# Kernel optimization log

Hardware: AMD Instinct MI355X
Metric: run time of the kernel (lower is better)

Reference implementation:

```python
import jax, jax.numpy as jnp
import numpy as np

EMBED_DIM = 768
N_HEADS = 12
HEAD_DIM = EMBED_DIM // N_HEADS


def setup_inputs() -> dict:
    key = jax.random.key(0)
    ks = jax.random.split(key, 5)
    B, T, C = 2, 4096, EMBED_DIM
    x = jax.random.normal(ks[0], (B, T, C), dtype=jnp.float32)
    # nn.Linear default init scale ~ 1/sqrt(fan_in); use small-scale normals
    s = 1.0 / np.sqrt(C)
    W_qkv = jax.random.normal(ks[1], (C, 3 * C), dtype=jnp.float32) * s
    b_qkv = jax.random.normal(ks[2], (3 * C,), dtype=jnp.float32) * s
    W_proj = jax.random.normal(ks[3], (C, C), dtype=jnp.float32) * s
    b_proj = jax.random.normal(ks[4], (C,), dtype=jnp.float32) * s
    return {"x": x, "W_qkv": W_qkv, "b_qkv": b_qkv, "W_proj": W_proj, "b_proj": b_proj}


def reference(x, W_qkv, b_qkv, W_proj, b_proj):
    B, T, C = x.shape
    H, D = N_HEADS, HEAD_DIM
    qkv = x @ W_qkv + b_qkv                      # [B,T,3C]
    q, k, v = jnp.split(qkv, 3, axis=2)
    # [B,T,C] -> [B,H,T,D]
    q = q.reshape(B, T, H, D).transpose(0, 2, 1, 3)
    k = k.reshape(B, T, H, D).transpose(0, 2, 1, 3)
    v = v.reshape(B, T, H, D).transpose(0, 2, 1, 3)
    scale = 1.0 / jnp.sqrt(jnp.float32(D)).astype(x.dtype)
    attn = jnp.einsum('bhtd,bhsd->bhts', q, k) * scale   # [B,H,T,T]
    causal = jnp.tril(jnp.ones((T, T), dtype=bool))
    attn = jnp.where(causal, attn, jnp.float32(-jnp.inf).astype(attn.dtype))
    attn = jax.nn.softmax(attn, axis=-1)
    # dropout p=0.0 -> identity
    out = jnp.einsum('bhts,bhsd->bhtd', attn, v)          # [B,H,T,D]
    out = out.transpose(0, 2, 1, 3).reshape(B, T, C)
    return out @ W_proj + b_proj
```

## Files before the change

### kernel.cpp

```cpp
#include <hip/hip_runtime.h>
#include <math.h>

#define T_SEQ 4096
#define CDIM  768
#define NH    12
#define HD    64
#define BATCH 2
#define MROWS (BATCH * T_SEQ)
#define N3C   (3 * CDIM)
#define HEADS_TOTAL (BATCH * NH)
#define QKV_ELEMS   ((size_t)HEADS_TOTAL * T_SEQ * HD)

#define QSCALE 0.18033688011112042f
#define SSHIFT -12.0f

typedef __bf16 bf16x8 __attribute__((ext_vector_type(8)));
typedef __bf16 bf16x4 __attribute__((ext_vector_type(4)));
typedef __bf16 bf16x2 __attribute__((ext_vector_type(2)));
typedef float  f32x4  __attribute__((ext_vector_type(4)));
typedef short  s16x4  __attribute__((ext_vector_type(4)));

union b4u { bf16x4 h; s16x4 s; };
__device__ __forceinline__ s16x4 as_s16(bf16x4 v) { b4u u; u.h = v; return u.s; }

typedef __attribute__((address_space(1))) const void as1_cvoid;
typedef __attribute__((address_space(3))) void as3_void;

__device__ __forceinline__ void gl16(const void* g, void* l) {
  __builtin_amdgcn_global_load_lds((as1_cvoid*)g, (as3_void*)l, 16, 0, 0);
}

__global__ __launch_bounds__(256) void cast_x_kernel(
    const float* __restrict__ x, __bf16* __restrict__ xb) {
  int i = (blockIdx.x * 256 + threadIdx.x) * 8;
  float4 a = *(const float4*)&x[i];
  float4 b = *(const float4*)&x[i + 4];
  bf16x8 o;
  o[0] = (__bf16)a.x; o[1] = (__bf16)a.y; o[2] = (__bf16)a.z; o[3] = (__bf16)a.w;
  o[4] = (__bf16)b.x; o[5] = (__bf16)b.y; o[6] = (__bf16)b.z; o[7] = (__bf16)b.w;
  *(bf16x8*)&xb[i] = o;
}

__global__ __launch_bounds__(256) void tcast_kernel(
    const float* __restrict__ W, __bf16* __restrict__ Wt, int K, int N) {
  __shared__ float tile[64][65];
  const int t  = threadIdx.x;
  const int k0 = blockIdx.y * 64, n0 = blockIdx.x * 64;
  const int r  = t >> 4, c4 = (t & 15) << 2;
#pragma unroll
  for (int i = 0; i < 4; ++i) {
    float4 v = *(const float4*)&W[(size_t)(k0 + r + i * 16) * N + n0 + c4];
    tile[r + i * 16][c4 + 0] = v.x; tile[r + i * 16][c4 + 1] = v.y;
    tile[r + i * 16][c4 + 2] = v.z; tile[r + i * 16][c4 + 3] = v.w;
  }
  __syncthreads();
#pragma unroll
  for (int i = 0; i < 4; ++i) {
    int nr = r + i * 16;
    bf16x4 o;
    o[0] = (__bf16)tile[c4 + 0][nr]; o[1] = (__bf16)tile[c4 + 1][nr];
    o[2] = (__bf16)tile[c4 + 2][nr]; o[3] = (__bf16)tile[c4 + 3][nr];
    *(bf16x4*)&Wt[(size_t)(n0 + nr) * K + k0 + c4] = o;
  }
}

__device__ __forceinline__ void mm_loop(const __bf16* __restrict__ A,
                                        const __bf16* __restrict__ Bt,
                                        int m0, int n0, __bf16* smem,
                                        f32x4 acc[4][4]) {
  const int t = threadIdx.x, wv = t >> 6, lane = t & 63;
  const int g2 = lane >> 4, c = lane & 15;
  __bf16* At = smem;
  __bf16* Bs = smem + 4096;
  const int ch0 = wv * 64 + lane;
  const int ch1 = 256 + ch0;
  const __bf16* gA0 = A  + (size_t)(m0 + (ch0 >> 2)) * CDIM + ((ch0 & 3) << 3);
  const __bf16* gA1 = A  + (size_t)(m0 + (ch1 >> 2)) * CDIM + ((ch1 & 3) << 3);
  const __bf16* gB0 = Bt + (size_t)(n0 + (ch0 >> 2)) * CDIM + ((ch0 & 3) << 3);
  const __bf16* gB1 = Bt + (size_t)(n0 + (ch1 >> 2)) * CDIM + ((ch1 & 3) << 3);
  __bf16* lA0 = At + (size_t)(wv * 64) * 8;
  __bf16* lA1 = At + (size_t)(256 + wv * 64) * 8;
  __bf16* lB0 = Bs + (size_t)(wv * 64) * 8;
  __bf16* lB1 = Bs + (size_t)(256 + wv * 64) * 8;
  const int mw = (wv & 1) << 6, nw = (wv >> 1) << 6;

  for (int kk = 0; kk < CDIM / 32; ++kk) {
    __syncthreads();
    gl16(gA0, lA0); gl16(gA1, lA1);
    gl16(gB0, lB0); gl16(gB1, lB1);
    gA0 += 32; gA1 += 32; gB0 += 32; gB1 += 32;
    __syncthreads();
    bf16x8 af[4], bfr[4];
#pragma unroll
    for (int mq = 0; mq < 4; ++mq)
      af[mq] = *(const bf16x8*)&At[(size_t)(mw + mq * 16 + c) * 32 + (g2 << 3)];
#pragma unroll
    for (int nq = 0; nq < 4; ++nq)
      bfr[nq] = *(const bf16x8*)&Bs[(size_t)(nw + nq * 16 + c) * 32 + (g2 << 3)];
#pragma unroll
    for (int mq = 0; mq < 4; ++mq)
#pragma unroll
      for (int nq = 0; nq < 4; ++nq)
        acc[mq][nq] = __builtin_amdgcn_mfma_f32_16x16x32_bf16(
            af[mq], bfr[nq], acc[mq][nq], 0, 0, 0);
  }
  __syncthreads();
}

__global__ __launch_bounds__(256) void qkv_mm_kernel(
    const __bf16* __restrict__ xb, const __bf16* __restrict__ Wt,
    const float* __restrict__ bias, __bf16* __restrict__ Qw,
    __bf16* __restrict__ Kw, __bf16* __restrict__ Vtw) {
  __shared__ __align__(16) __bf16 smem[18432];
  f32x4 acc[4][4];
#pragma unroll
  for (int i = 0; i < 4; ++i)
#pragma unroll
    for (int j = 0; j < 4; ++j) acc[i][j] = (f32x4){0.f, 0.f, 0.f, 0.f};

  const int m0 = blockIdx.y * 128, n0 = blockIdx.x * 128;
  mm_loop(xb, Wt, m0, n0, smem, acc);

  const int t = threadIdx.x, wv = t >> 6, lane = t & 63;
  const int g2 = lane >> 4, c = lane & 15;
  const int sel = n0 / CDIM;
  const int nn0 = n0 - sel * CDIM;
  const int h   = (nn0 >> 6) + (wv >> 1);
  const int mbase = m0 + ((wv & 1) << 6);
  const int b = mbase >> 12, tp0 = mbase & 4095;
  const int bh = b * NH + h;
  __bf16* Ep = smem + wv * 4608;
  float bcol[4];
#pragma unroll
  for (int nq = 0; nq < 4; ++nq)
    bcol[nq] = bias[n0 + ((wv >> 1) << 6) + nq * 16 + c];

  const int r8 = lane >> 3, c8 = (lane & 7) << 3;
  if (sel < 2) {
    const float scl = (sel == 0) ? QSCALE : 1.0f;
#pragma unroll
    for (int mq = 0; mq < 4; ++mq)
#pragma unroll
      for (int nq = 0; nq < 4; ++nq)
#pragma unroll
        for (int r = 0; r < 4; ++r)
          Ep[(size_t)(mq * 16 + (g2 << 2) + r) * 72 + nq * 16 + c] =
              (__bf16)((acc[mq][nq][r] + bcol[nq]) * scl);
    asm volatile("s_waitcnt lgkmcnt(0)" ::: "memory");
    __bf16* dst = (sel == 0) ? Qw : Kw;
#pragma unroll
    for (int p = 0; p < 8; ++p) {
      int row = p * 8 + r8;
      bf16x8 v = *(const bf16x8*)&Ep[(size_t)row * 72 + c8];
      *(bf16x8*)&dst[((size_t)bh * T_SEQ + tp0 + row) * HD + c8] = v;
    }
  } else {
#pragma unroll
    for (int mq = 0; mq < 4; ++mq)
#pragma unroll
      for (int nq = 0; nq < 4; ++nq)
#pragma unroll
        for (int r = 0; r < 4; ++r)
          Ep[(size_t)(nq * 16 + c) * 72 + mq * 16 + (g2 << 2) + r] =
              (__bf16)(acc[mq][nq][r] + bcol[nq]);
    asm volatile("s_waitcnt lgkmcnt(0)" ::: "memory");
#pragma unroll
    for (int p = 0; p < 8; ++p) {
      int d = p * 8 + r8;
      bf16x8 v = *(const bf16x8*)&Ep[(size_t)d * 72 + c8];
      *(bf16x8*)&Vtw[((size_t)bh * HD + d) * T_SEQ + tp0 + c8] = v;
    }
  }
}

struct Stage { bf16x8 k0, k1, v0, v1; };

__device__ __forceinline__ void issue_stage(const __bf16* __restrict__ Kb,
                                            const __bf16* __restrict__ Vb,
                                            int kt, int wv, int lane, Stage& sg) {
  const int r8 = lane >> 3;
  const int cc = (lane & 7) << 3;
  const int row0 = (wv << 4) + r8;
  const int row1 = row0 + 8;
  sg.k0 = *(const bf16x8*)&Kb[(size_t)(kt * 64 + row0) * HD + cc];
  sg.k1 = *(const bf16x8*)&Kb[(size_t)(kt * 64 + row1) * HD + cc];
  sg.v0 = *(const bf16x8*)&Vb[(size_t)row0 * T_SEQ + kt * 64 + cc];
  sg.v1 = *(const bf16x8*)&Vb[(size_t)row1 * T_SEQ + kt * 64 + cc];
}

__device__ __forceinline__ void write_stage(__bf16 (*KT)[64], __bf16 (*VT)[64],
                                            int wv, int lane, const Stage& sg) {
  const int r8 = lane >> 3;
  const int cc = ((lane & 7) << 3) ^ (r8 << 3);
  const int row0 = (wv << 4) + r8;
  const int row1 = row0 + 8;
  *(bf16x8*)&KT[row0][cc] = sg.k0;
  *(bf16x8*)&KT[row1][cc] = sg.k1;
  *(bf16x8*)&VT[row0][cc] = sg.v0;
  *(bf16x8*)&VT[row1][cc] = sg.v1;
}

__global__ __launch_bounds__(256) void attn_kernel(
    const __bf16* __restrict__ Q, const __bf16* __restrict__ K,
    const __bf16* __restrict__ Vt, __bf16* __restrict__ O) {
  __shared__ __align__(16) __bf16 KT[2][64][64];
  __shared__ __align__(16) __bf16 VT[2][64][64];

  const int t    = threadIdx.x;
  const int wv   = t >> 6;
  const int lane = t & 63;
  const int g2   = lane >> 4;
  const int c    = lane & 15;
  const int bh   = blockIdx.x;
  const int qt   = 63 - (int)blockIdx.y;

  const __bf16* Qb = Q  + (size_t)bh * T_SEQ * HD;
  const __bf16* Kb = K  + (size_t)bh * T_SEQ * HD;
  const __bf16* Vb = Vt + (size_t)bh * HD * T_SEQ;
  const int b = bh / NH, hh = bh % NH;

  const int qw = qt * 64 + wv * 16;

  bf16x8 qf0 = *(const bf16x8*)&Qb[(size_t)(qw + c) * HD +      (g2 << 3)];
  bf16x8 qf1 = *(const bf16x8*)&Qb[(size_t)(qw + c) * HD + 32 + (g2 << 3)];

  f32x4 ot[4];
#pragma unroll
  for (int dt = 0; dt < 4; ++dt) ot[dt] = (f32x4){0.f, 0.f, 0.f, 0.f};
  f32x4 lacc = (f32x4){0.f, 0.f, 0.f, 0.f};

  Stage sg;
  issue_stage(Kb, Vb, 0, wv, lane, sg);
  write_stage(KT[0], VT[0], wv, lane, sg);
  __syncthreads();

  const int swz = (c & 7) << 3;

#pragma unroll 1
  for (int kt = 0; kt <= qt; ++kt) {
    const int cur = kt & 1;
    if (kt < qt) issue_stage(Kb, Vb, kt + 1, wv, lane, sg);

    f32x4 S[4];
#pragma unroll
    for (int st = 0; st < 4; ++st) {
      bf16x8 kfa = *(const bf16x8*)&KT[cur][st * 16 + c][(g2 << 3) ^ swz];
      bf16x8 kfb = *(const bf16x8*)&KT[cur][st * 16 + c][((g2 << 3) + 32) ^ swz];
      S[st] = (f32x4){SSHIFT, SSHIFT, SSHIFT, SSHIFT};
      S[st] = __builtin_amdgcn_mfma_f32_16x16x32_bf16(kfa, qf0, S[st], 0, 0, 0);
      S[st] = __builtin_amdgcn_mfma_f32_16x16x32_bf16(kfb, qf1, S[st], 0, 0, 0);
    }

    if (kt == qt) {
      const int qloc = (wv << 4) + c;
#pragma unroll
      for (int st = 0; st < 4; ++st)
#pragma unroll
        for (int r = 0; r < 4; ++r)
          if ((st << 4) + (g2 << 2) + r > qloc) S[st][r] = -INFINITY;
    }

    s16x4 pf[4];
#pragma unroll
    for (int st = 0; st < 4; ++st) {
      bf16x4 ph;
#pragma unroll
      for (int r = 0; r < 4; ++r) {
        float p = exp2f(S[st][r]);
        lacc[r] += p;
        ph[r] = (__bf16)p;
      }
      pf[st] = as_s16(ph);
    }

#pragma unroll
    for (int dt = 0; dt < 4; ++dt) {
#pragma unroll
      for (int st = 0; st < 4; ++st) {
        bf16x4 vh = *(const bf16x4*)&VT[cur][dt * 16 + c]
                                       [((st << 4) + (g2 << 2)) ^ swz];
        ot[dt] = __builtin_amdgcn_mfma_f32_16x16x16bf16_1k(
            as_s16(vh), pf[st], ot[dt], 0, 0, 0);
      }
    }

    if (kt < qt) write_stage(KT[cur ^ 1], VT[cur ^ 1], wv, lane, sg);
    __syncthreads();
  }

  float l = lacc[0] + lacc[1] + lacc[2] + lacc[3];
  l += __shfl_xor(l, 16);
  l += __shfl_xor(l, 32);
  const float inv = 1.f / l;
  __bf16* orow = O + ((size_t)(b * T_SEQ + qw + c)) * CDIM + hh * HD;
#pragma unroll
  for (int dt = 0; dt < 4; ++dt) {
    bf16x4 v;
    v[0] = (__bf16)(ot[dt][0] * inv); v[1] = (__bf16)(ot[dt][1] * inv);
    v[2] = (__bf16)(ot[dt][2] * inv); v[3] = (__bf16)(ot[dt][3] * inv);
    *(bf16x4*)&orow[dt * 16 + (g2 << 2)] = v;
  }
}

__global__ __launch_bounds__(256) void proj_mm_kernel(
    const __bf16* __restrict__ Ob, const __bf16* __restrict__ Wt,
    const float* __restrict__ bias, float* __restrict__ out) {
  __shared__ __align__(16) __bf16 smem[8192];
  f32x4 acc[4][4];
#pragma unroll
  for (int i = 0; i < 4; ++i)
#pragma unroll
    for (int j = 0; j < 4; ++j) acc[i][j] = (f32x4){0.f, 0.f, 0.f, 0.f};

  const int m0 = blockIdx.y * 128, n0 = blockIdx.x * 128;
  mm_loop(Ob, Wt, m0, n0, smem, acc);

  const int t = threadIdx.x, wv = t >> 6, lane = t & 63;
  const int g2 = lane >> 4, c = lane & 15;
  const int mb = m0 + ((wv & 1) << 6), nb = n0 + ((wv >> 1) << 6);
  float bcol[4];
#pragma unroll
  for (int nq = 0; nq < 4; ++nq) bcol[nq] = bias[nb + nq * 16 + c];
#pragma unroll
  for (int mq = 0; mq < 4; ++mq)
#pragma unroll
    for (int nq = 0; nq < 4; ++nq)
#pragma unroll
      for (int r = 0; r < 4; ++r)
        out[(size_t)(mb + mq * 16 + (g2 << 2) + r) * CDIM + nb + nq * 16 + c] =
            acc[mq][nq][r] + bcol[nq];
}

extern "C" void kernel_launch(void* const* d_in, const int* in_sizes, int n_in,
                              void* d_out, int out_size, void* d_ws, size_t ws_size,
                              hipStream_t stream) {
  (void)in_sizes; (void)n_in; (void)out_size; (void)ws_size;
  const float* x      = (const float*)d_in[0];
  const float* W_qkv  = (const float*)d_in[1];
  const float* b_qkv  = (const float*)d_in[2];
  const float* W_proj = (const float*)d_in[3];
  const float* b_proj = (const float*)d_in[4];
  float* out = (float*)d_out;

  __bf16* Qw     = (__bf16*)d_ws;
  __bf16* Kw     = Qw  + QKV_ELEMS;
  __bf16* Vtw    = Kw  + QKV_ELEMS;
  __bf16* Ob     = Vtw + QKV_ELEMS;
  __bf16* xb     = Ob  + QKV_ELEMS;
  __bf16* Wqkvt  = xb  + QKV_ELEMS;
  __bf16* Wprojt = Wqkvt + (size_t)CDIM * N3C;

  cast_x_kernel<<<MROWS * CDIM / 2048, 256, 0, stream>>>(x, xb);
  tcast_kernel<<<dim3(N3C / 64, CDIM / 64), 256, 0, stream>>>(
      W_qkv, Wqkvt, CDIM, N3C);
  tcast_kernel<<<dim3(CDIM / 64, CDIM / 64), 256, 0, stream>>>(
      W_proj, Wprojt, CDIM, CDIM);

  qkv_mm_kernel<<<dim3(N3C / 128, MROWS / 128), 256, 0, stream>>>(
      xb, Wqkvt, b_qkv, Qw, Kw, Vtw);

  attn_kernel<<<dim3(HEADS_TOTAL, 64), 256, 0, stream>>>(Qw, Kw, Vtw, Ob);

  proj_mm_kernel<<<dim3(CDIM / 128, MROWS / 128), 256, 0, stream>>>(
      Ob, Wprojt, b_proj, out);
}
```

Measured before the change: 263.7 us.

## Process two query tiles per attention block sharing K/V stages, use direct global-to-LDS loads

Each attention block now handles two adjacent 64-row query tiles (128 rows), so every K/V tile staged in LDS is reused by twice as many MFMAs, and the grid is halved. K/V staging switches from register round-trips to direct global-to-LDS loads via gl16, and exp2f becomes the hardware exp2 builtin. The block order is remapped so the heaviest blocks launch first. In exchange, register pressure and per-block work double and there are fewer blocks to balance across CUs.

```diff
diff --git a/kernel.cpp b/kernel.cpp
--- a/kernel.cpp
+++ b/kernel.cpp
@@ -173,31 +173,12 @@
   }
 }
 
-struct Stage { bf16x8 k0, k1, v0, v1; };
-
-__device__ __forceinline__ void issue_stage(const __bf16* __restrict__ Kb,
-                                            const __bf16* __restrict__ Vb,
-                                            int kt, int wv, int lane, Stage& sg) {
-  const int r8 = lane >> 3;
-  const int cc = (lane & 7) << 3;
-  const int row0 = (wv << 4) + r8;
-  const int row1 = row0 + 8;
-  sg.k0 = *(const bf16x8*)&Kb[(size_t)(kt * 64 + row0) * HD + cc];
-  sg.k1 = *(const bf16x8*)&Kb[(size_t)(kt * 64 + row1) * HD + cc];
-  sg.v0 = *(const bf16x8*)&Vb[(size_t)row0 * T_SEQ + kt * 64 + cc];
-  sg.v1 = *(const bf16x8*)&Vb[(size_t)row1 * T_SEQ + kt * 64 + cc];
-}
-
-__device__ __forceinline__ void write_stage(__bf16 (*KT)[64], __bf16 (*VT)[64],
-                                            int wv, int lane, const Stage& sg) {
-  const int r8 = lane >> 3;
-  const int cc = ((lane & 7) << 3) ^ (r8 << 3);
-  const int row0 = (wv << 4) + r8;
-  const int row1 = row0 + 8;
-  *(bf16x8*)&KT[row0][cc] = sg.k0;
-  *(bf16x8*)&KT[row1][cc] = sg.k1;
-  *(bf16x8*)&VT[row0][cc] = sg.v0;
-  *(bf16x8*)&VT[row1][cc] = sg.v1;
+__device__ __forceinline__ void stage_tile(const __bf16* gk, const __bf16* gv,
+                                           __bf16* ldsK, __bf16* ldsV) {
+  gl16(gk,              ldsK);
+  gl16(gk + 8 * HD,     ldsK + 8 * 64);
+  gl16(gv,              ldsV);
+  gl16(gv + 8 * T_SEQ,  ldsV + 8 * 64);
 }
 
 __global__ __launch_bounds__(256) void attn_kernel(
@@ -212,65 +193,83 @@
   const int g2   = lane >> 4;
   const int c    = lane & 15;
   const int bh   = blockIdx.x;
-  const int qt   = 63 - (int)blockIdx.y;
+  const int yb   = (int)blockIdx.y;
+  const int p    = (yb < 11) ? (31 - yb) : (yb - 11);
+  const int ktmax = 2 * p + 1;
 
   const __bf16* Qb = Q  + (size_t)bh * T_SEQ * HD;
   const __bf16* Kb = K  + (size_t)bh * T_SEQ * HD;
   const __bf16* Vb = Vt + (size_t)bh * HD * T_SEQ;
   const int b = bh / NH, hh = bh % NH;
 
-  const int qw = qt * 64 + wv * 16;
-
-  bf16x8 qf0 = *(const bf16x8*)&Qb[(size_t)(qw + c) * HD +      (g2 << 3)];
-  bf16x8 qf1 = *(const bf16x8*)&Qb[(size_t)(qw + c) * HD + 32 + (g2 << 3)];
-
-  f32x4 ot[4];
-#pragma unroll
-  for (int dt = 0; dt < 4; ++dt) ot[dt] = (f32x4){0.f, 0.f, 0.f, 0.f};
-  f32x4 lacc = (f32x4){0.f, 0.f, 0.f, 0.f};
-
-  Stage sg;
-  issue_stage(Kb, Vb, 0, wv, lane, sg);
-  write_stage(KT[0], VT[0], wv, lane, sg);
+  const int qlo = p * 128 + wv * 16;
+  const int qhi = qlo + 64;
+
+  bf16x8 ql0 = *(const bf16x8*)&Qb[(size_t)(qlo + c) * HD +      (g2 << 3)];
+  bf16x8 ql1 = *(const bf16x8*)&Qb[(size_t)(qlo + c) * HD + 32 + (g2 << 3)];
+  bf16x8 qh0 = *(const bf16x8*)&Qb[(size_t)(qhi + c) * HD +      (g2 << 3)];
+  bf16x8 qh1 = *(const bf16x8*)&Qb[(size_t)(qhi + c) * HD + 32 + (g2 << 3)];
+
+  f32x4 ol[4], oh[4];
+#pragma unroll
+  for (int dt = 0; dt < 4; ++dt) {
+    ol[dt] = (f32x4){0.f, 0.f, 0.f, 0.f};
+    oh[dt] = (f32x4){0.f, 0.f, 0.f, 0.f};
+  }
+  f32x4 lacl = (f32x4){0.f, 0.f, 0.f, 0.f};
+  f32x4 lach = (f32x4){0.f, 0.f, 0.f, 0.f};
+
+  const int rr = lane >> 3;
+  const int lc = ((lane & 7) ^ rr) << 3;
+  const __bf16* gk = Kb + (size_t)(wv * 16 + rr) * HD    + lc;
+  const __bf16* gv = Vb + (size_t)(wv * 16 + rr) * T_SEQ + lc;
+
+  stage_tile(gk, gv, &KT[0][wv * 16][0], &VT[0][wv * 16][0]);
+  gk += 64 * HD; gv += 64;
   __syncthreads();
 
-  const int swz = (c & 7) << 3;
+  const int swz  = (c & 7) << 3;
+  const int qloc = (wv << 4) + c;
+  const f32x4 SINIT = (f32x4){SSHIFT, SSHIFT, SSHIFT, SSHIFT};
 
 #pragma unroll 1
-  for (int kt = 0; kt <= qt; ++kt) {
+  for (int kt = 0; kt < ktmax; ++kt) {
     const int cur = kt & 1;
-    if (kt < qt) issue_stage(Kb, Vb, kt + 1, wv, lane, sg);
-
-    f32x4 S[4];
+    stage_tile(gk, gv, &KT[cur ^ 1][wv * 16][0], &VT[cur ^ 1][wv * 16][0]);
+    gk += 64 * HD; gv += 64;
+
+    f32x4 SL[4], SH[4];
 #pragma unroll
     for (int st = 0; st < 4; ++st) {
       bf16x8 kfa = *(const bf16x8*)&KT[cur][st * 16 + c][(g2 << 3) ^ swz];
-      bf16x8 kfb = *(const bf16x8*)&KT[cur][st * 16 + c][((g2 << 3) + 32) ^ swz];
-      S[st] = (f32x4){SSHIFT, SSHIFT, SSHIFT, SSHIFT};
-      S[st] = __builtin_amdgcn_mfma_f32_16x16x32_bf16(kfa, qf0, S[st], 0, 0, 0);
-      S[st] = __builtin_amdgcn_mfma_f32_16x16x32_bf16(kfb, qf1, S[st], 0, 0, 0);
-    }
-
-    if (kt == qt) {
-      const int qloc = (wv << 4) + c;
+      bf16x8 kfb = *(const bf16x8*)&KT[cur][st * 16 + c][((4 + g2) << 3) ^ swz];
+      SL[st] = __builtin_amdgcn_mfma_f32_16x16x32_bf16(kfa, ql0, SINIT, 0, 0, 0);
+      SL[st] = __builtin_amdgcn_mfma_f32_16x16x32_bf16(kfb, ql1, SL[st], 0, 0, 0);
+      SH[st] = __builtin_amdgcn_mfma_f32_16x16x32_bf16(kfa, qh0, SINIT, 0, 0, 0);
+      SH[st] = __builtin_amdgcn_mfma_f32_16x16x32_bf16(kfb, qh1, SH[st], 0, 0, 0);
+    }
+
+    if (kt == ktmax - 1) {
 #pragma unroll
       for (int st = 0; st < 4; ++st)
 #pragma unroll
         for (int r = 0; r < 4; ++r)
-          if ((st << 4) + (g2 << 2) + r > qloc) S[st][r] = -INFINITY;
-    }
-
-    s16x4 pf[4];
+          if ((st << 4) + (g2 << 2) + r > qloc) SL[st][r] = -INFINITY;
+    }
+
+    s16x4 pfl[4], pfh[4];
 #pragma unroll
     for (int st = 0; st < 4; ++st) {
-      bf16x4 ph;
+      bf16x4 phl, phh;
 #pragma unroll
       for (int r = 0; r < 4; ++r) {
-        float p = exp2f(S[st][r]);
-        lacc[r] += p;
-        ph[r] = (__bf16)p;
+        float pl = __builtin_amdgcn_exp2f(SL[st][r]);
+        float ph = __builtin_amdgcn_exp2f(SH[st][r]);
+        lacl[r] += pl; lach[r] += ph;
+        phl[r] = (__bf16)pl; phh[r] = (__bf16)ph;
       }
-      pf[st] = as_s16(ph);
+      pfl[st] = as_s16(phl);
+      pfh[st] = as_s16(phh);
     }
 
 #pragma unroll
@@ -279,26 +278,81 @@
       for (int st = 0; st < 4; ++st) {
         bf16x4 vh = *(const bf16x4*)&VT[cur][dt * 16 + c]
                                        [((st << 4) + (g2 << 2)) ^ swz];
-        ot[dt] = __builtin_amdgcn_mfma_f32_16x16x16bf16_1k(
-            as_s16(vh), pf[st], ot[dt], 0, 0, 0);
+        s16x4 vs = as_s16(vh);
+        ol[dt] = __builtin_amdgcn_mfma_f32_16x16x16bf16_1k(vs, pfl[st], ol[dt], 0, 0, 0);
+        oh[dt] = __builtin_amdgcn_mfma_f32_16x16x16bf16_1k(vs, pfh[st], oh[dt], 0, 0, 0);
       }
     }
-
-    if (kt < qt) write_stage(KT[cur ^ 1], VT[cur ^ 1], wv, lane, sg);
     __syncthreads();
   }
 
-  float l = lacc[0] + lacc[1] + lacc[2] + lacc[3];
-  l += __shfl_xor(l, 16);
-  l += __shfl_xor(l, 32);
-  const float inv = 1.f / l;
-  __bf16* orow = O + ((size_t)(b * T_SEQ + qw + c)) * CDIM + hh * HD;
-#pragma unroll
-  for (int dt = 0; dt < 4; ++dt) {
-    bf16x4 v;
-    v[0] = (__bf16)(ot[dt][0] * inv); v[1] = (__bf16)(ot[dt][1] * inv);
-    v[2] = (__bf16)(ot[dt][2] * inv); v[3] = (__bf16)(ot[dt][3] * inv);
-    *(bf16x4*)&orow[dt * 16 + (g2 << 2)] = v;
+  {
+    const int cur = ktmax & 1;
+    f32x4 SH[4];
+#pragma unroll
+    for (int st = 0; st < 4; ++st) {
+      bf16x8 kfa = *(const bf16x8*)&KT[cur][st * 16 + c][(g2 << 3) ^ swz];
+      bf16x8 kfb = *(const bf16x8*)&KT[cur][st * 16 + c][((4 + g2) << 3) ^ swz];
+      SH[st] = __builtin_amdgcn_mfma_f32_16x16x32_bf16(kfa, qh0, SINIT, 0, 0, 0);
+      SH[st] = __builtin_amdgcn_mfma_f32_16x16x32_bf16(kfb, qh1, SH[st], 0, 0, 0);
+    }
+#pragma unroll
+    for (int st = 0; st < 4; ++st)
+#pragma unroll
+      for (int r = 0; r < 4; ++r)
+        if ((st << 4) + (g2 << 2) + r > qloc) SH[st][r] = -INFINITY;
+
+    s16x4 pfh[4];
+#pragma unroll
+    for (int st = 0; st < 4; ++st) {
+      bf16x4 phh;
+#pragma unroll
+      for (int r = 0; r < 4; ++r) {
+        float ph = __builtin_amdgcn_exp2f(SH[st][r]);
+        lach[r] += ph;
+        phh[r] = (__bf16)ph;
+      }
+      pfh[st] = as_s16(phh);
+    }
+#pragma unroll
+    for (int dt = 0; dt < 4; ++dt) {
+#pragma unroll
+      for (int st = 0; st < 4; ++st) {
+        bf16x4 vh = *(const bf16x4*)&VT[cur][dt * 16 + c]
+                                       [((st << 4) + (g2 << 2)) ^ swz];
+        oh[dt] = __builtin_amdgcn_mfma_f32_16x16x16bf16_1k(as_s16(vh), pfh[st],
+                                                           oh[dt], 0, 0, 0);
+      }
+    }
+  }
+
+  {
+    float l = lacl[0] + lacl[1] + lacl[2] + lacl[3];
+    l += __shfl_xor(l, 16);
+    l += __shfl_xor(l, 32);
+    const float inv = 1.f / l;
+    __bf16* orow = O + ((size_t)(b * T_SEQ + qlo + c)) * CDIM + hh * HD;
+#pragma unroll
+    for (int dt = 0; dt < 4; ++dt) {
+      bf16x4 v;
+      v[0] = (__bf16)(ol[dt][0] * inv); v[1] = (__bf16)(ol[dt][1] * inv);
+      v[2] = (__bf16)(ol[dt][2] * inv); v[3] = (__bf16)(ol[dt][3] * inv);
+      *(bf16x4*)&orow[dt * 16 + (g2 << 2)] = v;
+    }
+  }
+  {
+    float l = lach[0] + lach[1] + lach[2] + lach[3];
+    l += __shfl_xor(l, 16);
+    l += __shfl_xor(l, 32);
+    const float inv = 1.f / l;
+    __bf16* orow = O + ((size_t)(b * T_SEQ + qhi + c)) * CDIM + hh * HD;
+#pragma unroll
+    for (int dt = 0; dt < 4; ++dt) {
+      bf16x4 v;
+      v[0] = (__bf16)(oh[dt][0] * inv); v[1] = (__bf16)(oh[dt][1] * inv);
+      v[2] = (__bf16)(oh[dt][2] * inv); v[3] = (__bf16)(oh[dt][3] * inv);
+      *(bf16x4*)&orow[dt * 16 + (g2 << 2)] = v;
+    }
   }
 }
 
@@ -359,7 +413,7 @@
   qkv_mm_kernel<<<dim3(N3C / 128, MROWS / 128), 256, 0, stream>>>(
       xb, Wqkvt, b_qkv, Qw, Kw, Vtw);
 
-  attn_kernel<<<dim3(HEADS_TOTAL, 64), 256, 0, stream>>>(Qw, Kw, Vtw, Ob);
+  attn_kernel<<<dim3(HEADS_TOTAL, 32), 256, 0, stream>>>(Qw, Kw, Vtw, Ob);
 
   proj_mm_kernel<<<dim3(CDIM / 128, MROWS / 128), 256, 0, stream>>>(
       Ob, Wprojt, b_proj, out);
```

Result: no change. 263.1 us (-0.3%).

## Pair causal query tiles per block and stage K/V via direct global-to-LDS loads

Applied to the files above, without the earlier changes.

Each attention block now processes two query tiles, p and 63-p, so every block does the same amount of causal work and the grid is halved. The register-staged K/V prefetch, with its separate write to LDS, is replaced by gl16 direct global-to-LDS loads into the double buffer. The XOR swizzle moves to the global source address. The code also switches to the raw exp2 builtin and hoists the S init constant. This is meant to remove the imbalance across causal tiles and the VGPR round trip, but with half as many blocks, occupancy and tail behaviour may change.

```diff
diff --git a/kernel.cpp b/kernel.cpp
--- a/kernel.cpp
+++ b/kernel.cpp
@@ -173,31 +173,105 @@
   }
 }
 
-struct Stage { bf16x8 k0, k1, v0, v1; };
-
-__device__ __forceinline__ void issue_stage(const __bf16* __restrict__ Kb,
-                                            const __bf16* __restrict__ Vb,
-                                            int kt, int wv, int lane, Stage& sg) {
-  const int r8 = lane >> 3;
-  const int cc = (lane & 7) << 3;
-  const int row0 = (wv << 4) + r8;
-  const int row1 = row0 + 8;
-  sg.k0 = *(const bf16x8*)&Kb[(size_t)(kt * 64 + row0) * HD + cc];
-  sg.k1 = *(const bf16x8*)&Kb[(size_t)(kt * 64 + row1) * HD + cc];
-  sg.v0 = *(const bf16x8*)&Vb[(size_t)row0 * T_SEQ + kt * 64 + cc];
-  sg.v1 = *(const bf16x8*)&Vb[(size_t)row1 * T_SEQ + kt * 64 + cc];
-}
-
-__device__ __forceinline__ void write_stage(__bf16 (*KT)[64], __bf16 (*VT)[64],
-                                            int wv, int lane, const Stage& sg) {
-  const int r8 = lane >> 3;
-  const int cc = ((lane & 7) << 3) ^ (r8 << 3);
-  const int row0 = (wv << 4) + r8;
-  const int row1 = row0 + 8;
-  *(bf16x8*)&KT[row0][cc] = sg.k0;
-  *(bf16x8*)&KT[row1][cc] = sg.k1;
-  *(bf16x8*)&VT[row0][cc] = sg.v0;
-  *(bf16x8*)&VT[row1][cc] = sg.v1;
+__device__ __forceinline__ void stage_tile(const __bf16* gk, const __bf16* gv,
+                                           __bf16* ldsK, __bf16* ldsV) {
+  gl16(gk,              ldsK);
+  gl16(gk + 8 * HD,     ldsK + 8 * 64);
+  gl16(gv,              ldsV);
+  gl16(gv + 8 * T_SEQ,  ldsV + 8 * 64);
+}
+
+__device__ __forceinline__ void attn_tile(
+    const __bf16* __restrict__ Qb, const __bf16* __restrict__ Kb,
+    const __bf16* __restrict__ Vb, __bf16* __restrict__ O,
+    int b, int hh, int qt, int wv, int lane, int g2, int c,
+    __bf16 (*KT)[64][64], __bf16 (*VT)[64][64]) {
+  const int qw = qt * 64 + wv * 16;
+
+  bf16x8 qf0 = *(const bf16x8*)&Qb[(size_t)(qw + c) * HD +      (g2 << 3)];
+  bf16x8 qf1 = *(const bf16x8*)&Qb[(size_t)(qw + c) * HD + 32 + (g2 << 3)];
+
+  f32x4 ot[4];
+#pragma unroll
+  for (int dt = 0; dt < 4; ++dt) ot[dt] = (f32x4){0.f, 0.f, 0.f, 0.f};
+  f32x4 lacc = (f32x4){0.f, 0.f, 0.f, 0.f};
+
+  const int rr = lane >> 3;
+  const int lc = ((lane & 7) ^ rr) << 3;
+  const __bf16* gk = Kb + (size_t)(wv * 16 + rr) * HD    + lc;
+  const __bf16* gv = Vb + (size_t)(wv * 16 + rr) * T_SEQ + lc;
+
+  stage_tile(gk, gv, &KT[0][wv * 16][0], &VT[0][wv * 16][0]);
+  gk += 64 * HD; gv += 64;
+  __syncthreads();
+
+  const int swz  = (c & 7) << 3;
+  const int qloc = (wv << 4) + c;
+  const f32x4 SINIT = (f32x4){SSHIFT, SSHIFT, SSHIFT, SSHIFT};
+
+#pragma unroll 1
+  for (int kt = 0; kt <= qt; ++kt) {
+    const int cur = kt & 1;
+    if (kt < qt) {
+      stage_tile(gk, gv, &KT[cur ^ 1][wv * 16][0], &VT[cur ^ 1][wv * 16][0]);
+      gk += 64 * HD; gv += 64;
+    }
+
+    f32x4 S[4];
+#pragma unroll
+    for (int st = 0; st < 4; ++st) {
+      bf16x8 kfa = *(const bf16x8*)&KT[cur][st * 16 + c][(g2 << 3) ^ swz];
+      bf16x8 kfb = *(const bf16x8*)&KT[cur][st * 16 + c][((4 + g2) << 3) ^ swz];
+      S[st] = __builtin_amdgcn_mfma_f32_16x16x32_bf16(kfa, qf0, SINIT, 0, 0, 0);
+      S[st] = __builtin_amdgcn_mfma_f32_16x16x32_bf16(kfb, qf1, S[st], 0, 0, 0);
+    }
+
+    if (kt == qt) {
+#pragma unroll
+      for (int st = 0; st < 4; ++st)
+#pragma unroll
+        for (int r = 0; r < 4; ++r)
+          if ((st << 4) + (g2 << 2) + r > qloc) S[st][r] = -INFINITY;
+    }
+
+    s16x4 pf[4];
+#pragma unroll
+    for (int st = 0; st < 4; ++st) {
+      bf16x4 ph;
+#pragma unroll
+      for (int r = 0; r < 4; ++r) {
+        float pl = __builtin_amdgcn_exp2f(S[st][r]);
+        lacc[r] += pl;
+        ph[r] = (__bf16)pl;
+      }
+      pf[st] = as_s16(ph);
+    }
+
+#pragma unroll
+    for (int dt = 0; dt < 4; ++dt) {
+#pragma unroll
+      for (int st = 0; st < 4; ++st) {
+        bf16x4 vh = *(const bf16x4*)&VT[cur][dt * 16 + c]
+                                       [((st << 4) + (g2 << 2)) ^ swz];
+        ot[dt] = __builtin_amdgcn_mfma_f32_16x16x16bf16_1k(as_s16(vh), pf[st],
+                                                           ot[dt], 0, 0, 0);
+      }
+    }
+    __syncthreads();
+  }
+
+  float l = lacc[0] + lacc[1] + lacc[2] + lacc[3];
+  l += __shfl_xor(l, 16);
+  l += __shfl_xor(l, 32);
+  const float inv = 1.f / l;
+  __bf16* orow = O + ((size_t)(b * T_SEQ + qw + c)) * CDIM + hh * HD;
+#pragma unroll
+  for (int dt = 0; dt < 4; ++dt) {
+    bf16x4 v;
+    v[0] = (__bf16)(ot[dt][0] * inv); v[1] = (__bf16)(ot[dt][1] * inv);
+    v[2] = (__bf16)(ot[dt][2] * inv); v[3] = (__bf16)(ot[dt][3] * inv);
+    *(bf16x4*)&orow[dt * 16 + (g2 << 2)] = v;
+  }
 }
 
 __global__ __launch_bounds__(256) void attn_kernel(
@@ -212,94 +286,15 @@
   const int g2   = lane >> 4;
   const int c    = lane & 15;
   const int bh   = blockIdx.x;
-  const int qt   = 63 - (int)blockIdx.y;
+  const int p    = (int)blockIdx.y;
 
   const __bf16* Qb = Q  + (size_t)bh * T_SEQ * HD;
   const __bf16* Kb = K  + (size_t)bh * T_SEQ * HD;
   const __bf16* Vb = Vt + (size_t)bh * HD * T_SEQ;
   const int b = bh / NH, hh = bh % NH;
 
-  const int qw = qt * 64 + wv * 16;
-
-  bf16x8 qf0 = *(const bf16x8*)&Qb[(size_t)(qw + c) * HD +      (g2 << 3)];
-  bf16x8 qf1 = *(const bf16x8*)&Qb[(size_t)(qw + c) * HD + 32 + (g2 << 3)];
-
-  f32x4 ot[4];
-#pragma unroll
-  for (int dt = 0; dt < 4; ++dt) ot[dt] = (f32x4){0.f, 0.f, 0.f, 0.f};
-  f32x4 lacc = (f32x4){0.f, 0.f, 0.f, 0.f};
-
-  Stage sg;
-  issue_stage(Kb, Vb, 0, wv, lane, sg);
-  write_stage(KT[0], VT[0], wv, lane, sg);
-  __syncthreads();
-
-  const int swz = (c & 7) << 3;
-
-#pragma unroll 1
-  for (int kt = 0; kt <= qt; ++kt) {
-    const int cur = kt & 1;
-    if (kt < qt) issue_stage(Kb, Vb, kt + 1, wv, lane, sg);
-
-    f32x4 S[4];
-#pragma unroll
-    for (int st = 0; st < 4; ++st) {
-      bf16x8 kfa = *(const bf16x8*)&KT[cur][st * 16 + c][(g2 << 3) ^ swz];
-      bf16x8 kfb = *(const bf16x8*)&KT[cur][st * 16 + c][((g2 << 3) + 32) ^ swz];
-      S[st] = (f32x4){SSHIFT, SSHIFT, SSHIFT, SSHIFT};
-      S[st] = __builtin_amdgcn_mfma_f32_16x16x32_bf16(kfa, qf0, S[st], 0, 0, 0);
-      S[st] = __builtin_amdgcn_mfma_f32_16x16x32_bf16(kfb, qf1, S[st], 0, 0, 0);
-    }
-
-    if (kt == qt) {
-      const int qloc = (wv << 4) + c;
-#pragma unroll
-      for (int st = 0; st < 4; ++st)
-#pragma unroll
-        for (int r = 0; r < 4; ++r)
-          if ((st << 4) + (g2 << 2) + r > qloc) S[st][r] = -INFINITY;
-    }
-
-    s16x4 pf[4];
-#pragma unroll
-    for (int st = 0; st < 4; ++st) {
-      bf16x4 ph;
-#pragma unroll
-      for (int r = 0; r < 4; ++r) {
-        float p = exp2f(S[st][r]);
-        lacc[r] += p;
-        ph[r] = (__bf16)p;
-      }
-      pf[st] = as_s16(ph);
-    }
-
-#pragma unroll
-    for (int dt = 0; dt < 4; ++dt) {
-#pragma unroll
-      for (int st = 0; st < 4; ++st) {
-        bf16x4 vh = *(const bf16x4*)&VT[cur][dt * 16 + c]
-                                       [((st << 4) + (g2 << 2)) ^ swz];
-        ot[dt] = __builtin_amdgcn_mfma_f32_16x16x16bf16_1k(
-            as_s16(vh), pf[st], ot[dt], 0, 0, 0);
-      }
-    }
-
-    if (kt < qt) write_stage(KT[cur ^ 1], VT[cur ^ 1], wv, lane, sg);
-    __syncthreads();
-  }
-
-  float l = lacc[0] + lacc[1] + lacc[2] + lacc[3];
-  l += __shfl_xor(l, 16);
-  l += __shfl_xor(l, 32);
-  const float inv = 1.f / l;
-  __bf16* orow = O + ((size_t)(b * T_SEQ + qw + c)) * CDIM + hh * HD;
-#pragma unroll
-  for (int dt = 0; dt < 4; ++dt) {
-    bf16x4 v;
-    v[0] = (__bf16)(ot[dt][0] * inv); v[1] = (__bf16)(ot[dt][1] * inv);
-    v[2] = (__bf16)(ot[dt][2] * inv); v[3] = (__bf16)(ot[dt][3] * inv);
-    *(bf16x4*)&orow[dt * 16 + (g2 << 2)] = v;
-  }
+  attn_tile(Qb, Kb, Vb, O, b, hh, p,      wv, lane, g2, c, KT, VT);
+  attn_tile(Qb, Kb, Vb, O, b, hh, 63 - p, wv, lane, g2, c, KT, VT);
 }
 
 __global__ __launch_bounds__(256) void proj_mm_kernel(
@@ -359,7 +354,7 @@
   qkv_mm_kernel<<<dim3(N3C / 128, MROWS / 128), 256, 0, stream>>>(
       xb, Wqkvt, b_qkv, Qw, Kw, Vtw);
 
-  attn_kernel<<<dim3(HEADS_TOTAL, 64), 256, 0, stream>>>(Qw, Kw, Vtw, Ob);
+  attn_kernel<<<dim3(HEADS_TOTAL, 32), 256, 0, stream>>>(Qw, Kw, Vtw, Ob);
 
   proj_mm_kernel<<<dim3(CDIM / 128, MROWS / 128), 256, 0, stream>>>(
       Ob, Wprojt, b_proj, out);
```

Measured after the change: 249.4 us. 1.06x faster.
